# Optimization experiments

Hardware: AMD Instinct MI355X
Metric: run time of the kernel (lower is better)

The kernel has to match this reference:

```python
import math
import jax, jax.numpy as jnp
import numpy as np

T, D = 1024, 7168
N = 128
A_Q, A_KV = 1536, 512
QK_NOPE, QK_ROPE, V_DIM = 128, 64, 128
QK_HEAD = QK_NOPE + QK_ROPE  # 192
PAD_H = 256                  # padded to multiple of 128 in attn_op
EPS = 1e-6
ROPE_THETA, FACTOR, ORIG_MAX = 10000.0, 40.0, 4096
BETA_FAST, BETA_SLOW = 32, 1


def _yarn_inv_freq():
    """DeepseekScalingRotaryEmbedding (yarn) inverse frequencies, static."""
    dim = QK_ROPE
    pos_freqs = ROPE_THETA ** (np.arange(0, dim, 2, dtype=np.float64) / dim)
    inv_extra = 1.0 / pos_freqs
    inv_inter = 1.0 / (FACTOR * pos_freqs)

    def corr_dim(n_rot):
        return dim * math.log(ORIG_MAX / (n_rot * 2 * math.pi)) / (2 * math.log(ROPE_THETA))

    low = max(math.floor(corr_dim(BETA_FAST)), 0)
    high = min(math.ceil(corr_dim(BETA_SLOW)), dim - 1)
    ramp = np.clip((np.arange(dim // 2, dtype=np.float64) - low) / max(high - low, 1e-3), 0.0, 1.0)
    mask = 1.0 - ramp  # 1 -> extrapolation, 0 -> interpolation
    inv = inv_inter * (1.0 - mask) + inv_extra * mask
    return jnp.asarray(inv, dtype=jnp.float32)

_INV_FREQ = _yarn_inv_freq()
# mscale ratio: yarn_get_mscale(FACTOR, mscale)/yarn_get_mscale(FACTOR, mscale_all_dim) == 1.0
_MSCALE = 1.0


def _apply_rope(positions, x):
    # x: [T, N, QK_ROPE], split (rotate-half) ordering
    ang = positions[:, None].astype(jnp.float32) * _INV_FREQ[None, :]  # [T, 32]
    cos = (jnp.cos(ang) * _MSCALE)[:, None, :]
    sin = (jnp.sin(ang) * _MSCALE)[:, None, :]
    x1, x2 = x[..., : QK_ROPE // 2], x[..., QK_ROPE // 2:]
    return jnp.concatenate([x1 * cos - x2 * sin, x2 * cos + x1 * sin], axis=-1)


def _rms_norm(x, scale):
    var = jnp.mean(x * x, axis=-1, keepdims=True)
    return x * jax.lax.rsqrt(var + EPS) * scale


def setup_inputs() -> dict:
    key = jax.random.key(0)
    ks = jax.random.split(key, 6)
    s = 0.02
    return {
        "x": jax.random.normal(ks[0], (T, D), jnp.float32),
        "positions": jnp.arange(T, dtype=jnp.int32),
        "w_q_down": jax.random.normal(ks[1], (D, A_Q), jnp.float32) * s,
        "q_norm_scale": jnp.ones((A_Q,), jnp.float32),
        "w_q_up": jax.random.normal(ks[2], (A_Q, N, QK_HEAD), jnp.float32) * s,
        "w_kv_down": jax.random.normal(ks[3], (D, A_KV + QK_ROPE), jnp.float32) * s,
        "kv_norm_scale": jnp.ones((A_KV,), jnp.float32),
        "w_kv_up": jax.random.normal(ks[4], (A_KV, N, QK_NOPE + V_DIM), jnp.float32) * s,
        "w_o": jax.random.normal(ks[5], (N, V_DIM, D), jnp.float32) * s,
    }


def reference(x, positions, w_q_down, q_norm_scale, w_q_up, w_kv_down,
              kv_norm_scale, w_kv_up, w_o):
    # ---- q path: down-proj -> RMSNorm -> up-proj -> split RoPE ----
    q_TA = jnp.einsum('td,da->ta', x, w_q_down)
    q_TA = _rms_norm(q_TA, q_norm_scale)
    q_TNH = jnp.einsum('ta,anh->tnh', q_TA, w_q_up)
    q_rope = _apply_rope(positions, q_TNH[..., QK_NOPE:])
    q_TNH = jnp.concatenate([q_TNH[..., :QK_NOPE], q_rope], axis=-1)
    q_TNH = q_TNH * (QK_HEAD ** -0.5)

    # ---- kv path: down-proj -> (rope slice | RMSNorm latent -> up-proj) ----
    kv_SA = jnp.einsum('sd,da->sa', x, w_kv_down)
    k_rope = _apply_rope(positions, kv_SA[..., A_KV:][:, None, :])  # [S,1,64]
    k_rope = jnp.broadcast_to(k_rope, (T, N, QK_ROPE))
    c_SA = _rms_norm(kv_SA[..., :A_KV], kv_norm_scale)
    kv_nope = jnp.einsum('sa,anh->snh', c_SA, w_kv_up)
    k_SNH = jnp.concatenate([kv_nope[..., :QK_NOPE], k_rope], axis=-1)
    v_SNH = kv_nope[..., QK_NOPE:]

    # ---- attention (prefill, causal); zero-pad of head dim does not change dots,
    # but sm_scale uses the PADDED dim (256) as in the original attn_op ----
    sm_scale = PAD_H ** -0.5
    logits = jnp.einsum('tnh,snh->nts', q_TNH, k_SNH) * sm_scale
    t_idx = jnp.arange(T)
    causal = t_idx[:, None] >= t_idx[None, :]  # [T, S]
    logits = jnp.where(causal[None, :, :], logits, jnp.float32(-1e30))
    probs = jax.nn.softmax(logits, axis=-1)
    out_TNH = jnp.einsum('nts,snh->tnh', probs, v_SNH)

    # ---- output projection ----
    o_TD = jnp.einsum('tnh,nhd->td', out_TNH, w_o)
    return o_TD
```

## Files before the change

kernel.cpp:

```cpp
#include <hip/hip_runtime.h>
#include <hip/hip_bf16.h>
#include <math.h>

typedef __attribute__((ext_vector_type(4))) float f32x4;
typedef __attribute__((ext_vector_type(8))) short bf16x8;
typedef __attribute__((ext_vector_type(4))) short bf16x4;

static __device__ __forceinline__ float bf2f(short u){
  unsigned int i = ((unsigned int)(unsigned short)u) << 16;
  return __builtin_bit_cast(float, i);
}
static __device__ __forceinline__ short f2bf(float f){
  unsigned int u = __builtin_bit_cast(unsigned int, f);
  u += 0x7FFFu + ((u >> 16) & 1u);
  return (short)(u >> 16);
}

#define GLD16(g, l) __builtin_amdgcn_global_load_lds(                         \
    (const __attribute__((address_space(1))) void*)(g),                       \
    (__attribute__((address_space(3))) void*)(l), 16, 0, 0)

template<typename CT, int SPLITS>
__global__ __launch_bounds__(256) void gemm_bt(const short* __restrict__ A,
                                               const short* __restrict__ BT,
                                               CT* __restrict__ C,
                                               float* __restrict__ P,
                                               int M, int N, int K)
{
  __shared__ __align__(16) short As[2][128*32];
  __shared__ __align__(16) short Bs[2][128*32];
  const int tid = threadIdx.x;
  const int f   = blockIdx.y * 8 + blockIdx.x;
  const int nwg = 8 * gridDim.y;
  const int cpx = nwg >> 3;
  const int t   = (f & 7) * cpx + (f >> 3);
  const int m0  = (t & 7) * 128;
  const int n0  = (t >> 3) * 128;
  const int w = tid >> 6, lane = tid & 63;
  const int wr = w >> 1, wc = w & 1;
  const int g = lane >> 4, l16 = lane & 15;

  const int Ks   = K / SPLITS;
  const int kbeg = blockIdx.z * Ks;
  const int kend = kbeg + Ks;

  const int sr = lane >> 2;
  const int kc = (lane & 3) << 3;
  const int arow0 = m0 + w*16 + sr;
  const int arow1 = m0 + (w+4)*16 + sr;
  int brow0 = n0 + w*16 + sr;      if (brow0 >= N) brow0 = N - 1;
  int brow1 = n0 + (w+4)*16 + sr;  if (brow1 >= N) brow1 = N - 1;
  const short* aG0 = A  + (size_t)arow0 * K + kc;
  const short* aG1 = A  + (size_t)arow1 * K + kc;
  const short* bG0 = BT + (size_t)brow0 * K + kc;
  const short* bG1 = BT + (size_t)brow1 * K + kc;
  char* aL = (char*)As;
  char* bL = (char*)Bs;

  auto stage = [&](int buf, int k0){
    char* ab = aL + buf*8192;
    char* bb = bL + buf*8192;
    GLD16(aG0 + k0, ab + (w  )*1024);
    GLD16(aG1 + k0, ab + (w+4)*1024);
    GLD16(bG0 + k0, bb + (w  )*1024);
    GLD16(bG1 + k0, bb + (w+4)*1024);
  };

  f32x4 acc[4][4];
  #pragma unroll
  for (int i=0;i<4;i++)
    #pragma unroll
    for (int j=0;j<4;j++) acc[i][j] = (f32x4){0.f,0.f,0.f,0.f};

  stage(0, kbeg);
  __syncthreads();

  int cur = 0;
  for (int k0 = kbeg; k0 < kend; k0 += 32){
    if (k0 + 32 < kend) stage(cur ^ 1, k0 + 32);

    const char* ar = aL + cur*8192;
    const char* br = bL + cur*8192;
    bf16x8 af[4], bfm[4];
    #pragma unroll
    for (int mi=0;mi<4;mi++){
      int row = wr*64 + mi*16 + l16;
      af[mi] = *reinterpret_cast<const bf16x8*>(ar + row*64 + g*16);
    }
    #pragma unroll
    for (int ni=0;ni<4;ni++){
      int row = wc*64 + ni*16 + l16;
      bfm[ni] = *reinterpret_cast<const bf16x8*>(br + row*64 + g*16);
    }
    #pragma unroll
    for (int mi=0;mi<4;mi++)
      #pragma unroll
      for (int ni=0;ni<4;ni++)
        acc[mi][ni] = __builtin_amdgcn_mfma_f32_16x16x32_bf16(af[mi], bfm[ni], acc[mi][ni], 0, 0, 0);

    __syncthreads();
    cur ^= 1;
  }

  #pragma unroll
  for (int mi=0;mi<4;mi++){
    int row = m0 + wr*64 + mi*16 + g*4;
    #pragma unroll
    for (int ni=0;ni<4;ni++){
      int col = n0 + wc*64 + ni*16 + l16;
      if (col < N){
        #pragma unroll
        for (int r=0;r<4;r++){
          if constexpr (SPLITS > 1){
            P[(size_t)blockIdx.z*M*N + (size_t)(row+r)*N + col] = acc[mi][ni][r];
          } else if constexpr (sizeof(CT) == 4){
            C[(size_t)(row+r)*N + col] = acc[mi][ni][r];
          } else {
            C[(size_t)(row+r)*N + col] = f2bf(acc[mi][ni][r]);
          }
        }
      }
    }
  }
}

template<int NP>
__global__ __launch_bounds__(256) void reduceN(const float* __restrict__ p,
                                               float* __restrict__ out,
                                               int n4, int mn4)
{
  int i = blockIdx.x * 256 + threadIdx.x;
  const int stride = gridDim.x * 256;
  for (; i < n4; i += stride){
    f32x4 s = reinterpret_cast<const f32x4*>(p)[i];
    #pragma unroll
    for (int z = 1; z < NP; z++)
      s = s + reinterpret_cast<const f32x4*>(p)[(size_t)z*mn4 + i];
    reinterpret_cast<f32x4*>(out)[i] = s;
  }
}

__global__ __launch_bounds__(256) void transpose_f32_bf16(const float* __restrict__ src,
                                                          short* __restrict__ dst,
                                                          int R, int C)
{
  __shared__ float tl[64][68];
  const int tid = threadIdx.x;
  const int r0 = blockIdx.y * 64, c0 = blockIdx.x * 64;
  {
    const int lr = tid >> 4, lc = (tid & 15) << 2;
    #pragma unroll
    for (int p = 0; p < 4; p++){
      int row = p*16 + lr;
      f32x4 v = *reinterpret_cast<const f32x4*>(src + (size_t)(r0+row)*C + c0 + lc);
      *reinterpret_cast<f32x4*>(&tl[row][lc]) = v;
    }
  }
  __syncthreads();
  {
    const int n = tid >> 2, ks = (tid & 3) << 4;
    short tmp[16];
    #pragma unroll
    for (int j = 0; j < 16; j++) tmp[j] = f2bf(tl[ks + j][n]);
    short* d = dst + (size_t)(c0+n)*R + r0 + ks;
    *reinterpret_cast<bf16x8*>(d)     = *reinterpret_cast<bf16x8*>(&tmp[0]);
    *reinterpret_cast<bf16x8*>(d + 8) = *reinterpret_cast<bf16x8*>(&tmp[8]);
  }
}

__global__ __launch_bounds__(256) void conv_f32_bf16(const float* __restrict__ src,
                                                     short* __restrict__ dst, int n4)
{
  int i = blockIdx.x * 256 + threadIdx.x;
  const int stride = gridDim.x * 256;
  for (; i < n4; i += stride){
    f32x4 v = reinterpret_cast<const f32x4*>(src)[i];
    bf16x4 h; h[0]=f2bf(v[0]); h[1]=f2bf(v[1]); h[2]=f2bf(v[2]); h[3]=f2bf(v[3]);
    reinterpret_cast<bf16x4*>(dst)[i] = h;
  }
}

__global__ __launch_bounds__(256) void mla_rmsnorm_bf(const float* __restrict__ dc,
                                                      const float* __restrict__ scale,
                                                      short* __restrict__ out)
{
  const int t = blockIdx.x;
  const float* row = dc + (size_t)t * 2112;
  float ss = 0.f;
  for (int i = threadIdx.x; i < 1536; i += 256){ float v = row[i]; ss += v*v; }
  #pragma unroll
  for (int off = 32; off >= 1; off >>= 1) ss += __shfl_xor(ss, off);
  __shared__ float red[4];
  if ((threadIdx.x & 63) == 0) red[threadIdx.x >> 6] = ss;
  __syncthreads();
  ss = red[0] + red[1] + red[2] + red[3];
  const float rs = 1.0f / sqrtf(ss / 1536.f + 1e-6f);
  for (int i = threadIdx.x; i < 1536; i += 256)
    out[(size_t)t*1536 + i] = f2bf(row[i] * rs * scale[i]);
}

__device__ __forceinline__ void yarn_cs(int pos, int j, float& c, float& s){
  const double dim = 64.0;
  double pf = pow(10000.0, (2.0*(double)j)/dim);
  double inv_extra = 1.0/pf;
  double inv_inter = inv_extra/40.0;
  double lo = floor(dim*log(4096.0/(32.0*2.0*M_PI))/(2.0*log(10000.0)));
  double hi = ceil (dim*log(4096.0/(       2.0*M_PI))/(2.0*log(10000.0)));
  if (lo < 0.0) lo = 0.0;
  if (hi > dim - 1.0) hi = dim - 1.0;
  double denom = hi - lo; if (denom < 0.001) denom = 0.001;
  double ramp = ((double)j - lo)/denom;
  ramp = ramp < 0.0 ? 0.0 : (ramp > 1.0 ? 1.0 : ramp);
  double mask = 1.0 - ramp;
  float invf = (float)(inv_inter*(1.0 - mask) + inv_extra*mask);
  float ang = (float)pos * invf;
  c = cosf(ang); s = sinf(ang);
}

__global__ __launch_bounds__(256) void mla_rope_q(short* __restrict__ qb,
                                                  const int* __restrict__ positions)
{
  const int t = blockIdx.x;
  __shared__ float cs[32], sn[32];
  if (threadIdx.x < 32){
    float c, s; yarn_cs(positions[t], threadIdx.x, c, s);
    cs[threadIdx.x] = c; sn[threadIdx.x] = s;
  }
  __syncthreads();
  const float f = 0.004510548978043951f;
  short* row = qb + (size_t)t * 24576;
  for (int idx = threadIdx.x; idx < 128*160; idx += 256){
    int n = idx / 160, e = idx % 160;
    short* p = row + n*192;
    if (e < 128){
      p[e] = f2bf(bf2f(p[e]) * f);
    } else {
      int j = e - 128;
      float x1 = bf2f(p[128+j]), x2 = bf2f(p[160+j]);
      p[128+j] = f2bf((x1*cs[j] - x2*sn[j]) * f);
      p[160+j] = f2bf((x2*cs[j] + x1*sn[j]) * f);
    }
  }
}

__global__ __launch_bounds__(256) void mla_kv_post(const float* __restrict__ dc,
                                                   const float* __restrict__ scale,
                                                   const int* __restrict__ positions,
                                                   short* __restrict__ cbuf,
                                                   short* __restrict__ krope)
{
  const int t = blockIdx.x;
  const float* row = dc + (size_t)t * 2112 + 1536;
  float ss = 0.f;
  for (int i = threadIdx.x; i < 512; i += 256){ float v = row[i]; ss += v*v; }
  #pragma unroll
  for (int off = 32; off >= 1; off >>= 1) ss += __shfl_xor(ss, off);
  __shared__ float red[4];
  if ((threadIdx.x & 63) == 0) red[threadIdx.x >> 6] = ss;
  __syncthreads();
  ss = red[0] + red[1] + red[2] + red[3];
  const float rs = 1.0f / sqrtf(ss / 512.f + 1e-6f);
  for (int i = threadIdx.x; i < 512; i += 256)
    cbuf[(size_t)t*512 + i] = f2bf(row[i] * rs * scale[i]);
  if (threadIdx.x < 32){
    int j = threadIdx.x;
    float c, s; yarn_cs(positions[t], j, c, s);
    float x1 = row[512 + j], x2 = row[544 + j];
    krope[(size_t)t*64 + j]      = f2bf(x1*c - x2*s);
    krope[(size_t)t*64 + 32 + j] = f2bf(x2*c + x1*s);
  }
}

__global__ __launch_bounds__(512) void mla_attn2(const short* __restrict__ qb,
                                                 const short* __restrict__ kvup,
                                                 const short* __restrict__ krope,
                                                 short* __restrict__ attn_out)
{
  const int f = blockIdx.x;
  const int xcd = f & 7, pos = f >> 3;
  const int n  = xcd*16 + (pos >> 2);
  const int pair = pos & 3;
  const int tid = threadIdx.x, w = tid >> 6, lane = tid & 63;
  const int g = lane >> 4, l16 = lane & 15;

  __shared__ __align__(16) short Klds[64*192];
  __shared__ __align__(16) short Vlds[128*64];
  __shared__ __align__(16) short Plds[8][16*64];
  char* KB = (char*)Klds; char* VB = (char*)Vlds; char* PB = (char*)Plds[w];

  bf16x8 kpre[3], vpre[2];

  int kS[3], kHB[3];
  #pragma unroll
  for (int c=0;c<3;c++){
    int lin = c*512 + tid;
    kS[c] = lin / 24; kHB[c] = (lin % 24) * 8;
  }
  int vS[2], vVB[2], vROT[2];
  #pragma unroll
  for (int c=0;c<2;c++){
    int lin = c*512 + tid;
    vS[c] = lin >> 4; vVB[c] = (lin & 15) << 3; vROT[c] = (lin & 15) & 7;
  }

  auto stage_load = [&](int S0){
    #pragma unroll
    for (int c=0;c<3;c++){
      const short* src = (kHB[c] < 128)
        ? kvup  + (size_t)(S0 + kS[c])*32768 + n*256 + kHB[c]
        : krope + (size_t)(S0 + kS[c])*64 + (kHB[c]-128);
      kpre[c] = *reinterpret_cast<const bf16x8*>(src);
    }
    #pragma unroll
    for (int c=0;c<2;c++)
      vpre[c] = *reinterpret_cast<const bf16x8*>(kvup + (size_t)(S0 + vS[c])*32768 + n*256 + 128 + vVB[c]);
  };
  auto stage_write = [&](){
    #pragma unroll
    for (int c=0;c<3;c++){
      unsigned byte = (unsigned)(kS[c]*384 + kHB[c]*2) ^ ((unsigned)(kS[c]&7)<<4);
      *reinterpret_cast<bf16x8*>(KB + byte) = kpre[c];
    }
    #pragma unroll
    for (int c=0;c<2;c++){
      #pragma unroll
      for (int i=0;i<8;i++){
        int v = vVB[c] + i;
        unsigned byte = (unsigned)(v*128 + ((vS[c]*2 + vROT[c]*16) & 127));
        *reinterpret_cast<short*>(VB + byte) = vpre[c][i];
      }
    }
  };

  stage_load(0);
  stage_write();
  __syncthreads();

  #pragma unroll
  for (int p = 0; p < 2; p++){
    const int qtl = p ? (7 - pair) : pair;
    const int t0 = qtl * 128;
    const int last = 2*qtl + 1;

    bf16x8 qf[6];
    {
      const size_t qrow = (size_t)(t0 + w*16 + l16) * 24576 + (size_t)n * 192;
      #pragma unroll
      for (int c=0;c<6;c++)
        qf[c] = *reinterpret_cast<const bf16x8*>(qb + qrow + c*32 + g*8);
    }
    f32x4 o[8];
    #pragma unroll
    for (int i=0;i<8;i++) o[i] = (f32x4){0.f,0.f,0.f,0.f};
    float m[4], l[4];
    #pragma unroll
    for (int r=0;r<4;r++){ m[r] = -1e30f; l[r] = 0.f; }

    for (int sb = 0; sb <= last; sb++){
      const bool more = (sb < last) || (p == 0);
      if (more) stage_load((sb < last) ? (sb+1)*64 : 0);

      f32x4 S[4];
      __builtin_amdgcn_s_setprio(1);
      #pragma unroll
      for (int st=0; st<4; st++){
        f32x4 sacc = (f32x4){0.f,0.f,0.f,0.f};
        int srow = st*16 + l16;
        #pragma unroll
        for (int c=0;c<6;c++){
          unsigned byte = (unsigned)(srow*384 + c*64 + g*16) ^ ((unsigned)(srow&7)<<4);
          bf16x8 kf = *reinterpret_cast<const bf16x8*>(KB + byte);
          sacc = __builtin_amdgcn_mfma_f32_16x16x32_bf16(qf[c], kf, sacc, 0, 0, 0);
        }
        S[st] = sacc;
      }
      __builtin_amdgcn_s_setprio(0);

      if (sb >= 2*qtl){
        #pragma unroll
        for (int st=0;st<4;st++){
          int sg = sb*64 + st*16 + l16;
          #pragma unroll
          for (int r=0;r<4;r++){
            int qg = t0 + w*16 + g*4 + r;
            if (sg > qg) S[st][r] = -1e30f;
          }
        }
      }
      float alpha[4];
      #pragma unroll
      for (int r=0;r<4;r++){
        float mx = fmaxf(fmaxf(S[0][r],S[1][r]), fmaxf(S[2][r],S[3][r]));
        #pragma unroll
        for (int off=8; off>=1; off>>=1) mx = fmaxf(mx, __shfl_xor(mx, off));
        float mnew = fmaxf(m[r], mx);
        alpha[r] = __expf(m[r] - mnew);
        m[r] = mnew;
        l[r] *= alpha[r];
      }
      #pragma unroll
      for (int st=0;st<4;st++)
        #pragma unroll
        for (int r=0;r<4;r++)
          S[st][r] = __expf(S[st][r] - m[r]);
      #pragma unroll
      for (int r=0;r<4;r++){
        float sum = S[0][r]+S[1][r]+S[2][r]+S[3][r];
        #pragma unroll
        for (int off=8; off>=1; off>>=1) sum += __shfl_xor(sum, off);
        l[r] += sum;
      }
      #pragma unroll
      for (int vt=0; vt<8; vt++)
        #pragma unroll
        for (int r=0;r<4;r++) o[vt][r] *= alpha[r];

      #pragma unroll
      for (int st=0;st<4;st++){
        #pragma unroll
        for (int r=0;r<4;r++){
          int qrow = g*4 + r, scol = st*16 + l16;
          unsigned byte = (unsigned)(qrow*128 + scol*2) ^ ((unsigned)(qrow&7)<<4);
          *reinterpret_cast<short*>(PB + byte) = f2bf(S[st][r]);
        }
      }
      bf16x8 pf[2];
      #pragma unroll
      for (int c=0;c<2;c++){
        unsigned byte = (unsigned)(l16*128 + (c*32 + g*8)*2) ^ ((unsigned)(l16&7)<<4);
        pf[c] = *reinterpret_cast<const bf16x8*>(PB + byte);
      }
      __builtin_amdgcn_s_setprio(1);
      #pragma unroll
      for (int vt=0; vt<8; vt++){
        #pragma unroll
        for (int c=0;c<2;c++){
          int vrow = vt*16 + l16;
          int rot = (vrow >> 3) & 7;
          unsigned byte = (unsigned)(vrow*128 + ((c*64 + g*16 + rot*16) & 127));
          bf16x8 vf = *reinterpret_cast<const bf16x8*>(VB + byte);
          o[vt] = __builtin_amdgcn_mfma_f32_16x16x32_bf16(pf[c], vf, o[vt], 0, 0, 0);
        }
      }
      __builtin_amdgcn_s_setprio(0);

      if (more){
        __syncthreads();
        stage_write();
        __syncthreads();
      }
    }

    #pragma unroll
    for (int r=0;r<4;r++){
      float inv = 1.f / l[r];
      int t = t0 + w*16 + g*4 + r;
      #pragma unroll
      for (int vt=0;vt<8;vt++){
        int v = vt*16 + l16;
        attn_out[(size_t)t*16384 + n*128 + v] = f2bf(o[vt][r] * inv);
      }
    }
  }
}

extern "C" void kernel_launch(void* const* d_in, const int* in_sizes, int n_in,
                              void* d_out, int out_size, void* d_ws, size_t ws_size,
                              hipStream_t stream) {
  const float* x            = (const float*)d_in[0];
  const int*   positions    = (const int*)  d_in[1];
  const float* w_q_down     = (const float*)d_in[2];
  const float* q_norm_scale = (const float*)d_in[3];
  const float* w_q_up       = (const float*)d_in[4];
  const float* w_kv_down    = (const float*)d_in[5];
  const float* kv_norm_scale= (const float*)d_in[6];
  const float* w_kv_up      = (const float*)d_in[7];
  const float* w_o          = (const float*)d_in[8];

  char* p = (char*)d_ws;
  short* xbf   = (short*)p; p += (size_t)1024*7168*2;
  short* wdT   = (short*)p; p += (size_t)2112*7168*2;
  short* wquT  = (short*)p; p += (size_t)24576*1536*2;
  short* wkuT  = (short*)p; p += (size_t)32768*512*2;
  short* woT   = (short*)p; p += (size_t)7168*16384*2;
  float* downC = (float*)p; p += (size_t)1024*2112*4;
  short* qAbf  = (short*)p; p += (size_t)1024*1536*2;
  short* q_b   = (short*)p; p += (size_t)1024*24576*2;
  short* cbuf  = (short*)p; p += (size_t)1024*512*2;
  short* krope = (short*)p; p += (size_t)1024*64*2;
  short* kvup  = (short*)p; p += (size_t)1024*32768*2;
  short* attn_o= (short*)p; p += (size_t)1024*16384*2;

  float* pDown = (float*)q_b;
  float* pWo   = (float*)d_ws;

  dim3 blk(256);
  conv_f32_bf16<<<2048, blk, 0, stream>>>(x, xbf, 1024*7168/4);
  transpose_f32_bf16<<<dim3(24, 112),  blk, 0, stream>>>(w_q_down,  wdT,                     7168, 1536);
  transpose_f32_bf16<<<dim3(9, 112),   blk, 0, stream>>>(w_kv_down, wdT + (size_t)1536*7168, 7168, 576);
  transpose_f32_bf16<<<dim3(384, 24),  blk, 0, stream>>>(w_q_up,    wquT,                    1536, 24576);
  transpose_f32_bf16<<<dim3(512, 8),   blk, 0, stream>>>(w_kv_up,   wkuT,                    512,  32768);
  transpose_f32_bf16<<<dim3(112, 256), blk, 0, stream>>>(w_o,       woT,                     16384, 7168);

  gemm_bt<float, 4><<<dim3(8, 17, 4), blk, 0, stream>>>(xbf, wdT, (float*)nullptr, pDown, 1024, 2112, 7168);
  reduceN<4><<<1024, blk, 0, stream>>>(pDown, downC, 1024*2112/4, 1024*2112/4);
  mla_rmsnorm_bf<<<1024, blk, 0, stream>>>(downC, q_norm_scale, qAbf);
  mla_kv_post<<<1024, blk, 0, stream>>>(downC, kv_norm_scale, positions, cbuf, krope);

  gemm_bt<short, 1><<<dim3(8, 192), blk, 0, stream>>>(qAbf, wquT, q_b, nullptr, 1024, 24576, 1536);
  mla_rope_q<<<1024, blk, 0, stream>>>(q_b, positions);
  gemm_bt<short, 1><<<dim3(8, 256), blk, 0, stream>>>(cbuf, wkuT, kvup, nullptr, 1024, 32768, 512);

  mla_attn2<<<512, dim3(512), 0, stream>>>(q_b, kvup, krope, attn_o);

  gemm_bt<float, 2><<<dim3(8, 56, 2), blk, 0, stream>>>(attn_o, woT, (float*)nullptr, pWo, 1024, 7168, 16384);
  reduceN<2><<<2048, blk, 0, stream>>>(pWo, (float*)d_out, 1024*7168/4, 1024*7168/4);
}
```

Baseline: 975.0 us.

## Add 256x256-tile 4-stage pipelined GEMM for up-projection and output GEMMs

Adds a new 512-thread GEMM kernel with 256x256 output tiles, a 4-deep global-to-LDS pipeline in 128KB of dynamic shared memory, swizzled LDS reads and s_setprio around the MFMA block. It replaces the 128x128 gemm_bt for the q up-projection, kv up-projection and split-K output projection. The larger tiles are meant to raise arithmetic intensity and cut global and LDS traffic, and the deeper prefetch is meant to hide load latency. In exchange it uses more registers and LDS per block, which lowers occupancy, and it launches fewer blocks, which can leave CUs idle on the smaller GEMMs.

```diff
diff --git a/kernel.cpp b/kernel.cpp
--- a/kernel.cpp
+++ b/kernel.cpp
@@ -19,6 +19,121 @@
 #define GLD16(g, l) __builtin_amdgcn_global_load_lds(                         \
     (const __attribute__((address_space(1))) void*)(g),                       \
     (__attribute__((address_space(3))) void*)(l), 16, 0, 0)
+
+template<typename CT, int SPLITS>
+__global__ __launch_bounds__(512, 2) void gemm256(const short* __restrict__ A,
+                                                  const short* __restrict__ BT,
+                                                  CT* __restrict__ C,
+                                                  float* __restrict__ P,
+                                                  int M, int N, int K)
+{
+  extern __shared__ __align__(16) char smem[];
+  const int tid = threadIdx.x;
+  const int w = tid >> 6, lane = tid & 63;
+  const int wm = w >> 2, wn = w & 3;
+  const int g = lane >> 4, l16 = lane & 15;
+
+  const int per_z = gridDim.x * gridDim.y;
+  const int F = (blockIdx.z * gridDim.y + blockIdx.y) * gridDim.x + blockIdx.x;
+  const int nwgF = per_z * gridDim.z;
+  const int cpxF = nwgF >> 3;
+  const int T = (F & 7) * cpxF + (F >> 3);
+  const int zz = T / per_z, tt = T % per_z;
+  const int m0 = (tt & 3) * 256;
+  const int n0 = (tt >> 2) * 256;
+
+  const int Ks   = K / SPLITS;
+  const int kbeg = zz * Ks;
+  const int NT   = Ks >> 5;
+
+  const int gg = (lane & 3) ^ ((lane >> 2) & 3) ^ ((lane >> 4) & 1);
+  const short* aSrc[2]; const short* bSrc[2];
+  int ldsOff[2];
+  #pragma unroll
+  for (int j = 0; j < 2; j++){
+    int r = (w + j*8)*16 + (lane >> 2);
+    aSrc[j] = A  + (size_t)(m0 + r) * K + kbeg + gg*8;
+    bSrc[j] = BT + (size_t)(n0 + r) * K + kbeg + gg*8;
+    ldsOff[j] = (w + j*8) * 1024;
+  }
+
+  const int sw = ((g ^ (l16 & 3) ^ ((l16 >> 2) & 1)) << 4);
+
+  f32x4 acc[8][4];
+  #pragma unroll
+  for (int i = 0; i < 8; i++)
+    #pragma unroll
+    for (int j = 0; j < 4; j++) acc[i][j] = (f32x4){0.f,0.f,0.f,0.f};
+
+  auto stage = [&](int b, int t){
+    const int koff = t * 32;
+    char* dst = smem + b * 32768;
+    #pragma unroll
+    for (int j = 0; j < 2; j++){
+      GLD16(aSrc[j] + koff, dst + ldsOff[j]);
+      GLD16(bSrc[j] + koff, dst + 16384 + ldsOff[j]);
+    }
+  };
+
+  auto wait_pub = [&](int ahead){
+    if (ahead >= 3)      asm volatile("s_waitcnt vmcnt(8)" ::: "memory");
+    else if (ahead == 2) asm volatile("s_waitcnt vmcnt(4)" ::: "memory");
+    else                 asm volatile("s_waitcnt vmcnt(0)" ::: "memory");
+    __builtin_amdgcn_s_barrier();
+    asm volatile("" ::: "memory");
+  };
+
+  stage(0, 0);
+  if (NT > 1) stage(1, 1);
+  if (NT > 2) stage(2, 2);
+  wait_pub(NT - 1 >= 2 ? (NT > 2 ? 3 : 2) : 1);
+
+  const int arow = wm*128 + l16;
+  const int brow = wn*64  + l16;
+
+  for (int t = 0; t < NT; t++){
+    const int sl = t & 3;
+    if (t + 3 < NT) stage((t + 3) & 3, t + 3);
+
+    const char* base = smem + sl * 32768;
+    bf16x8 a[8], bb[4];
+    #pragma unroll
+    for (int mi = 0; mi < 8; mi++)
+      a[mi] = *reinterpret_cast<const bf16x8*>(base + (arow + mi*16)*64 + sw);
+    #pragma unroll
+    for (int ni = 0; ni < 4; ni++)
+      bb[ni] = *reinterpret_cast<const bf16x8*>(base + 16384 + (brow + ni*16)*64 + sw);
+
+    __builtin_amdgcn_s_setprio(1);
+    #pragma unroll
+    for (int mi = 0; mi < 8; mi++)
+      #pragma unroll
+      for (int ni = 0; ni < 4; ni++)
+        acc[mi][ni] = __builtin_amdgcn_mfma_f32_16x16x32_bf16(a[mi], bb[ni], acc[mi][ni], 0, 0, 0);
+    __builtin_amdgcn_s_setprio(0);
+
+    wait_pub(NT - 1 - t);
+  }
+
+  #pragma unroll
+  for (int mi = 0; mi < 8; mi++){
+    int row = m0 + wm*128 + mi*16 + g*4;
+    #pragma unroll
+    for (int ni = 0; ni < 4; ni++){
+      int col = n0 + wn*64 + ni*16 + l16;
+      #pragma unroll
+      for (int r = 0; r < 4; r++){
+        if constexpr (SPLITS > 1){
+          P[(size_t)zz*M*N + (size_t)(row+r)*N + col] = acc[mi][ni][r];
+        } else if constexpr (sizeof(CT) == 4){
+          C[(size_t)(row+r)*N + col] = acc[mi][ni][r];
+        } else {
+          C[(size_t)(row+r)*N + col] = f2bf(acc[mi][ni][r]);
+        }
+      }
+    }
+  }
+}
 
 template<typename CT, int SPLITS>
 __global__ __launch_bounds__(256) void gemm_bt(const short* __restrict__ A,
@@ -494,6 +609,11 @@
   float* pDown = (float*)q_b;
   float* pWo   = (float*)d_ws;
 
+  hipFuncSetAttribute(reinterpret_cast<const void*>(&gemm256<short,1>),
+                      hipFuncAttributeMaxDynamicSharedMemorySize, 131072);
+  hipFuncSetAttribute(reinterpret_cast<const void*>(&gemm256<float,2>),
+                      hipFuncAttributeMaxDynamicSharedMemorySize, 131072);
+
   dim3 blk(256);
   conv_f32_bf16<<<2048, blk, 0, stream>>>(x, xbf, 1024*7168/4);
   transpose_f32_bf16<<<dim3(24, 112),  blk, 0, stream>>>(w_q_down,  wdT,                     7168, 1536);
@@ -507,12 +627,12 @@
   mla_rmsnorm_bf<<<1024, blk, 0, stream>>>(downC, q_norm_scale, qAbf);
   mla_kv_post<<<1024, blk, 0, stream>>>(downC, kv_norm_scale, positions, cbuf, krope);
 
-  gemm_bt<short, 1><<<dim3(8, 192), blk, 0, stream>>>(qAbf, wquT, q_b, nullptr, 1024, 24576, 1536);
+  gemm256<short, 1><<<dim3(4, 96), dim3(512), 131072, stream>>>(qAbf, wquT, q_b, nullptr, 1024, 24576, 1536);
   mla_rope_q<<<1024, blk, 0, stream>>>(q_b, positions);
-  gemm_bt<short, 1><<<dim3(8, 256), blk, 0, stream>>>(cbuf, wkuT, kvup, nullptr, 1024, 32768, 512);
+  gemm256<short, 1><<<dim3(4, 128), dim3(512), 131072, stream>>>(cbuf, wkuT, kvup, nullptr, 1024, 32768, 512);
 
   mla_attn2<<<512, dim3(512), 0, stream>>>(q_b, kvup, krope, attn_o);
 
-  gemm_bt<float, 2><<<dim3(8, 56, 2), blk, 0, stream>>>(attn_o, woT, (float*)nullptr, pWo, 1024, 7168, 16384);
+  gemm256<float, 2><<<dim3(4, 28, 2), dim3(512), 131072, stream>>>(attn_o, woT, (float*)nullptr, pWo, 1024, 7168, 16384);
   reduceN<2><<<2048, blk, 0, stream>>>(pWo, (float*)d_out, 1024*7168/4, 1024*7168/4);
 }
```

Measured after the change: 883.1 us. 9.4% less time.
